# Kernel tuning notes

Hardware: AMD Instinct MI355X
Metric: run time of the kernel (lower is better)

## Reference

```python
import jax, jax.numpy as jnp
import numpy as np

B, S, M = 32, 512, 8
DF = 512          # per-feature dim (face/fc/img/label)
DIM1 = 4 * DF     # 2048
DIM2 = 512        # memory dim / hidden dim
EPS = 1e-05


def setup_inputs() -> dict:
    key = jax.random.key(0)
    ks = jax.random.split(key, 10)
    def g(k, shape, scale=1.0):
        return jax.random.normal(k, shape, dtype=jnp.float32) * scale
    fc_feat = g(ks[0], (B, S, DF))
    img_feat = g(ks[1], (B, S, DF))
    label_feat = g(ks[2], (B, DF))
    memory = g(ks[3], (B, M, DIM2))
    face = g(ks[4], (B, S, DF))
    face_mask = jax.random.randint(ks[5], (B, S), 0, 2).astype(jnp.float32)
    # params: linear1 (dim1+dim2 -> dim2) with bias, linear2 (dim2 -> 1) no bias
    xav1 = (2.0 / (DIM1 + DIM2 + DIM2)) ** 0.5
    xav2 = (2.0 / (DIM2 + 1)) ** 0.5
    W1 = g(ks[6], (DIM2, DIM1 + DIM2), xav1)
    b1 = jnp.zeros((DIM2,), dtype=jnp.float32)
    w2 = g(ks[7], (DIM2,), xav2)
    return {"fc_feat": fc_feat, "img_feat": img_feat, "label_feat": label_feat,
            "memory": memory, "face": face, "face_mask": face_mask,
            "W1": W1, "b1": b1, "w2": w2}


def reference(fc_feat, img_feat, label_feat, memory, face, face_mask, W1, b1, w2):
    b, s, _ = face.shape
    m = memory.shape[1]
    # concat along feature dim of (face, fc, img, label) -> [B,S,DIM1]
    base = jnp.concatenate(
        [face, fc_feat, img_feat,
         jnp.broadcast_to(label_feat[:, None, :], (b, s, label_feat.shape[-1]))],
        axis=-1)
    # linear1 split: W1 @ cat(base, mem) = W1a@base + W1b@mem  (avoids B*M*S*(dim1+dim2) concat)
    part_base = jnp.einsum('bsd,hd->bsh', base, W1[:, :DIM1])      # [B,S,H]
    part_mem = jnp.einsum('bmd,hd->bmh', memory, W1[:, DIM1:])     # [B,M,H]
    h = jnp.tanh(part_base[:, None, :, :] + part_mem[:, :, None, :] + b1)  # [B,M,S,H]
    e = jnp.einsum('bmsh,h->bms', h, w2).reshape(b, m * s)         # memory-major flatten
    alpha = jax.nn.softmax(e, axis=1)
    final_mask = jnp.tile(face_mask, (1, m))                       # face_mask.repeat(1, M)
    alpha = alpha * final_mask
    alpha = alpha / (alpha.sum(axis=1, keepdims=True) + EPS)
    # bmm(alpha, face.repeat(1,M,1)) == sum over m,s of alpha * face
    context = jnp.einsum('bms,bsd->bd', alpha.reshape(b, m, s), face)
    return alpha, context
```

## Files before the change

### kernel.cpp

```cpp
#include <hip/hip_runtime.h>
#include <hip/hip_bf16.h>
#include <math.h>

#define NB 32
#define NS 512
#define NM 8
#define NH 512
#define WSTRIDE 2560
#define FEPS 1e-5f

typedef __attribute__((ext_vector_type(4))) float f32x4;
typedef __attribute__((ext_vector_type(8))) short bf16x8;
typedef __attribute__((ext_vector_type(8))) unsigned short ushort8;

__device__ __forceinline__ unsigned short f2b(float f) {
  union { __hip_bfloat16 h; unsigned short u; } cv;
  cv.h = __float2bfloat16(f);
  return cv.u;
}

#define LDSK 40

template<int KSTEPS>
__global__ __launch_bounds__(256, 4)
void gemm_base_kernel(const float* __restrict__ face,
                      const float* __restrict__ fcf,
                      const float* __restrict__ imgf,
                      const float* __restrict__ labf,
                      const float* __restrict__ W1,
                      float* __restrict__ pb)
{
  __shared__ unsigned short As[2][128 * LDSK];
  __shared__ unsigned short Bs[2][128 * LDSK];

  const int tid  = threadIdx.x;
  const int lane = tid & 63;
  const int wid  = tid >> 6;
  const int wr   = wid >> 1;
  const int wc   = wid & 1;

  const int bid = blockIdx.x;
  const int cpx = gridDim.x >> 3;
  const int sid = (bid & 7) * cpx + (bid >> 3);
  const int kk   = sid >> 9;
  const int blkm = (sid >> 2) & 127;
  const int blkn = sid & 3;

  const int r  = tid >> 1;
  const int ch = (tid & 1) << 4;

  const int gr = blkm * 128 + r;
  const int bb = gr >> 9;
  const int gh = blkn * 128 + r;

  const int rl = lane & 15;
  const int kq = (lane >> 4) << 3;

  f32x4 acc[4][4];
  #pragma unroll
  for (int i = 0; i < 4; ++i)
    #pragma unroll
    for (int j = 0; j < 4; ++j)
      acc[i][j] = (f32x4){0.f, 0.f, 0.f, 0.f};

  float ra[16], rb[16];

#define LOAD_REGS(KTG) do {                                                 \
    const int kt_ = (KTG);                                                  \
    const int off_ = ((kt_ & 15) << 5) | ch;                                \
    const int reg_ = kt_ >> 4;                                              \
    const float* pa_;                                                       \
    if      (reg_ == 0) pa_ = face + (size_t)gr * 512 + off_;               \
    else if (reg_ == 1) pa_ = fcf  + (size_t)gr * 512 + off_;               \
    else if (reg_ == 2) pa_ = imgf + (size_t)gr * 512 + off_;               \
    else                pa_ = labf + (size_t)bb * 512 + off_;               \
    const float* pw_ = W1 + (size_t)gh * WSTRIDE + (kt_ << 5) + ch;         \
    _Pragma("unroll")                                                       \
    for (int i_ = 0; i_ < 4; ++i_) {                                        \
      f32x4 va_ = *(const f32x4*)(pa_ + 4 * i_);                            \
      f32x4 vb_ = *(const f32x4*)(pw_ + 4 * i_);                            \
      ra[4*i_+0] = va_[0]; ra[4*i_+1] = va_[1];                             \
      ra[4*i_+2] = va_[2]; ra[4*i_+3] = va_[3];                             \
      rb[4*i_+0] = vb_[0]; rb[4*i_+1] = vb_[1];                             \
      rb[4*i_+2] = vb_[2]; rb[4*i_+3] = vb_[3];                             \
    }                                                                       \
  } while (0)

#define WRITE_LDS(BUF) do {                                                 \
    ushort8 a0_, a1_, b0_, b1_;                                             \
    _Pragma("unroll")                                                       \
    for (int j_ = 0; j_ < 8; ++j_) {                                        \
      a0_[j_] = f2b(ra[j_]);   a1_[j_] = f2b(ra[8 + j_]);                   \
      b0_[j_] = f2b(rb[j_]);   b1_[j_] = f2b(rb[8 + j_]);                   \
    }                                                                       \
    *(ushort8*)&As[BUF][r * LDSK + ch]     = a0_;                           \
    *(ushort8*)&As[BUF][r * LDSK + ch + 8] = a1_;                           \
    *(ushort8*)&Bs[BUF][r * LDSK + ch]     = b0_;                           \
    *(ushort8*)&Bs[BUF][r * LDSK + ch + 8] = b1_;                           \
  } while (0)

#define COMPUTE(BUF) do {                                                   \
    bf16x8 af_[4], bf_[4];                                                  \
    _Pragma("unroll")                                                       \
    for (int m_ = 0; m_ < 4; ++m_)                                          \
      af_[m_] = *(const bf16x8*)&As[BUF][(wr*64 + m_*16 + rl) * LDSK + kq]; \
    _Pragma("unroll")                                                       \
    for (int n_ = 0; n_ < 4; ++n_)                                          \
      bf_[n_] = *(const bf16x8*)&Bs[BUF][(wc*64 + n_*16 + rl) * LDSK + kq]; \
    _Pragma("unroll")                                                       \
    for (int m_ = 0; m_ < 4; ++m_)                                          \
      _Pragma("unroll")                                                     \
      for (int n_ = 0; n_ < 4; ++n_)                                        \
        acc[m_][n_] = __builtin_amdgcn_mfma_f32_16x16x32_bf16(              \
            af_[m_], bf_[n_], acc[m_][n_], 0, 0, 0);                        \
  } while (0)

  const int kbase = kk * 32;
  LOAD_REGS(kbase);
  WRITE_LDS(0);
  __syncthreads();

  int buf = 0;
  #pragma unroll 1
  for (int kt = 0; kt < KSTEPS; ++kt) {
    if (kt < KSTEPS - 1) LOAD_REGS(kbase + kt + 1);
    COMPUTE(buf);
    if (kt < KSTEPS - 1) WRITE_LDS(buf ^ 1);
    __syncthreads();
    buf ^= 1;
  }

  float* pbo = pb + (size_t)kk * ((size_t)NB * NS * 512);
  const int crow = blkm * 128 + wr * 64;
  const int ccol = blkn * 128 + wc * 64 + rl;
  #pragma unroll
  for (int m = 0; m < 4; ++m)
    #pragma unroll
    for (int n = 0; n < 4; ++n)
      #pragma unroll
      for (int j = 0; j < 4; ++j) {
        const int row = crow + m * 16 + (lane >> 4) * 4 + j;
        pbo[(size_t)row * 512 + ccol + n * 16] = acc[m][n][j];
      }

#undef LOAD_REGS
#undef WRITE_LDS
#undef COMPUTE
}

__global__ __launch_bounds__(256)
void pm_kernel(const float* __restrict__ memory,
               const float* __restrict__ W1,
               const float* __restrict__ b1,
               float* __restrict__ pm)
{
  __shared__ float ms[NM * 512];
  const int b  = blockIdx.x;
  const int ht = blockIdx.y;
  const int t  = threadIdx.x;
  const int w  = t >> 6;
  const int l  = t & 63;

  const float* src = memory + (size_t)b * NM * 512;
  #pragma unroll
  for (int i = 0; i < 4; ++i)
    ((f32x4*)ms)[t + i * 256] = ((const f32x4*)src)[t + i * 256];
  __syncthreads();

  #pragma unroll 1
  for (int i = 0; i < 16; ++i) {
    const int h = ht * 64 + w * 16 + i;
    const float* wrow = W1 + (size_t)h * WSTRIDE + 2048;
    const f32x4 w0 = *(const f32x4*)(wrow + l * 4);
    const f32x4 w1 = *(const f32x4*)(wrow + 256 + l * 4);
    float part[NM];
    #pragma unroll
    for (int m = 0; m < NM; ++m) {
      const f32x4 m0 = *(const f32x4*)&ms[m * 512 + l * 4];
      const f32x4 m1 = *(const f32x4*)&ms[m * 512 + 256 + l * 4];
      part[m] = w0[0]*m0[0] + w0[1]*m0[1] + w0[2]*m0[2] + w0[3]*m0[3]
              + w1[0]*m1[0] + w1[1]*m1[1] + w1[2]*m1[2] + w1[3]*m1[3];
    }
    #pragma unroll
    for (int off = 32; off >= 1; off >>= 1)
      #pragma unroll
      for (int m = 0; m < NM; ++m)
        part[m] += __shfl_xor(part[m], off);
    if (l == 0) {
      const float bias = b1[h];
      #pragma unroll
      for (int m = 0; m < NM; ++m)
        pm[((size_t)b * NM + m) * 512 + h] = part[m] + bias;
    }
  }
}

template<int SPLIT>
__global__ __launch_bounds__(128)
void e_kernel(const float* __restrict__ pb0,
              const float* __restrict__ pb1,
              const float* __restrict__ pm,
              const float* __restrict__ w2,
              float* __restrict__ e)
{
  __shared__ float pbs[16 * 516];
  __shared__ float pms[NM * 516];
  __shared__ float w2s[512];

  const int b  = blockIdx.x;
  const int st = blockIdx.y;
  const int t  = threadIdx.x;

  const f32x4* s0 = (const f32x4*)(pb0 + ((size_t)b * NS + st * 16) * 512);
  const f32x4* s1 = (const f32x4*)(pb1 + ((size_t)b * NS + st * 16) * 512);
  #pragma unroll
  for (int i = 0; i < 16; ++i) {
    const int fi = t + i * 128;
    f32x4 v = s0[fi];
    if (SPLIT) {
      f32x4 v1 = s1[fi];
      v[0]+=v1[0]; v[1]+=v1[1]; v[2]+=v1[2]; v[3]+=v1[3];
    }
    const int f32i = fi * 4;
    *(f32x4*)&pbs[(f32i >> 9) * 516 + (f32i & 511)] = v;
  }
  const float* pmsrc = pm + (size_t)b * NM * 512;
  #pragma unroll
  for (int i = 0; i < 8; ++i) {
    const int fi = t + i * 128;
    f32x4 v = ((const f32x4*)pmsrc)[fi];
    const int f32i = fi * 4;
    *(f32x4*)&pms[(f32i >> 9) * 516 + (f32i & 511)] = v;
  }
  ((f32x4*)w2s)[t] = ((const f32x4*)w2)[t];
  __syncthreads();

  const int sl = t >> 3;
  const int m  = t & 7;
  const float* prow = &pbs[sl * 516];
  const float* mrow = &pms[m * 516];

  float acc = 0.f;
  for (int h = 0; h < 512; h += 4) {
    f32x4 pv = *(const f32x4*)&prow[h];
    f32x4 mv = *(const f32x4*)&mrow[h];
    f32x4 wv = *(const f32x4*)&w2s[h];
    #pragma unroll
    for (int j = 0; j < 4; ++j) {
      const float x  = pv[j] + mv[j];
      const float ex = __expf(x + x);
      const float th = 1.f - __fdividef(2.f, ex + 1.f);
      acc += wv[j] * th;
    }
  }
  e[(size_t)b * (NM * NS) + m * NS + st * 16 + sl] = acc;
}

__global__ __launch_bounds__(256)
void softmax_kernel(const float* __restrict__ e,
                    const float* __restrict__ face_mask,
                    float* __restrict__ out_alpha,
                    float* __restrict__ wsum)
{
  __shared__ float ev[NM * NS];
  __shared__ float msk[NS];
  __shared__ float redX[4], redA[4], redM[4];

  const int b = blockIdx.x;
  const int t = threadIdx.x;
  const int lane = t & 63;
  const int wv = t >> 6;

  const float* erow = e + (size_t)b * (NM * NS);
  #pragma unroll
  for (int i = 0; i < 4; ++i)
    ((f32x4*)ev)[t + i * 256] = ((const f32x4*)erow)[t + i * 256];
  if (t < 128)
    ((f32x4*)msk)[t] = ((const f32x4*)(face_mask + (size_t)b * NS))[t];
  __syncthreads();

  float mx = -3.402823466e38f;
  for (int i = t; i < NM * NS; i += 256) mx = fmaxf(mx, ev[i]);
  #pragma unroll
  for (int o = 32; o >= 1; o >>= 1) mx = fmaxf(mx, __shfl_xor(mx, o));
  if (lane == 0) redX[wv] = mx;
  __syncthreads();
  mx = fmaxf(fmaxf(redX[0], redX[1]), fmaxf(redX[2], redX[3]));

  float sA = 0.f, sM = 0.f;
  for (int i = t; i < NM * NS; i += 256) {
    const float p = __expf(ev[i] - mx);
    ev[i] = p;
    sA += p;
    sM += p * msk[i & 511];
  }
  #pragma unroll
  for (int o = 32; o >= 1; o >>= 1) {
    sA += __shfl_xor(sA, o);
    sM += __shfl_xor(sM, o);
  }
  if (lane == 0) { redA[wv] = sA; redM[wv] = sM; }
  __syncthreads();
  sA = redA[0] + redA[1] + redA[2] + redA[3];
  sM = redM[0] + redM[1] + redM[2] + redM[3];

  const float rr = sM / sA;
  const float scale = 1.f / (sA * (rr + FEPS));

  for (int i = t; i < NM * NS; i += 256) {
    const float a = ev[i] * msk[i & 511] * scale;
    ev[i] = a;
    out_alpha[(size_t)b * (NM * NS) + i] = a;
  }
  __syncthreads();

  for (int s = t; s < NS; s += 256) {
    float w = 0.f;
    #pragma unroll
    for (int m = 0; m < NM; ++m) w += ev[m * NS + s];
    wsum[(size_t)b * NS + s] = w;
  }
}

__global__ __launch_bounds__(128)
void ctx_kernel(const float* __restrict__ wsum,
                const float* __restrict__ face,
                float* __restrict__ out_ctx)
{
  const int b  = blockIdx.x;
  const int sq = blockIdx.y;
  const int t  = threadIdx.x;

  f32x4 acc = (f32x4){0.f, 0.f, 0.f, 0.f};
  const int s0 = sq * 64;
  #pragma unroll 4
  for (int si = 0; si < 64; ++si) {
    const int s = s0 + si;
    const float w = wsum[(size_t)b * NS + s];
    const f32x4 fv = ((const f32x4*)(face + ((size_t)b * NS + s) * 512))[t];
    acc[0] += w * fv[0]; acc[1] += w * fv[1];
    acc[2] += w * fv[2]; acc[3] += w * fv[3];
  }
  float* dst = out_ctx + (size_t)b * 512 + t * 4;
  atomicAdd(dst + 0, acc[0]);
  atomicAdd(dst + 1, acc[1]);
  atomicAdd(dst + 2, acc[2]);
  atomicAdd(dst + 3, acc[3]);
}

extern "C" void kernel_launch(void* const* d_in, const int* in_sizes, int n_in,
                              void* d_out, int out_size, void* d_ws, size_t ws_size,
                              hipStream_t stream)
{
  const float* fc_feat  = (const float*)d_in[0];
  const float* img_feat = (const float*)d_in[1];
  const float* label    = (const float*)d_in[2];
  const float* memory   = (const float*)d_in[3];
  const float* face     = (const float*)d_in[4];
  const float* fmask    = (const float*)d_in[5];
  const float* W1       = (const float*)d_in[6];
  const float* b1       = (const float*)d_in[7];
  const float* w2       = (const float*)d_in[8];

  float* out       = (float*)d_out;
  float* alpha_out = out;
  float* ctx_out   = out + (size_t)NB * NM * NS;

  const size_t szPB = (size_t)NB * NS * 512 * 4;
  const size_t szPM = (size_t)NB * NM * 512 * 4;
  const size_t szE  = (size_t)NB * NM * NS * 4;
  const size_t need_split = 2 * szPB + szPM + szE + (size_t)NB * NS * 4;
  const bool split = ws_size >= need_split;

  char* ws = (char*)d_ws;
  float* pb0 = (float*)ws;
  float* pb1 = split ? (float*)(ws + szPB) : pb0;
  char*  tail = ws + (split ? 2 * szPB : szPB);
  float* pm = (float*)tail;
  float* ee = (float*)(tail + szPM);
  float* wsum = (float*)(tail + szPM + szE);

  hipMemsetAsync(ctx_out, 0, (size_t)NB * 512 * 4, stream);

  if (split)
    gemm_base_kernel<32><<<1024, 256, 0, stream>>>(face, fc_feat, img_feat, label, W1, pb0);
  else
    gemm_base_kernel<64><<<512, 256, 0, stream>>>(face, fc_feat, img_feat, label, W1, pb0);

  pm_kernel<<<dim3(NB, 8), 256, 0, stream>>>(memory, W1, b1, pm);

  if (split)
    e_kernel<1><<<dim3(NB, NS / 16), 128, 0, stream>>>(pb0, pb1, pm, w2, ee);
  else
    e_kernel<0><<<dim3(NB, NS / 16), 128, 0, stream>>>(pb0, pb1, pm, w2, ee);

  softmax_kernel<<<NB, 256, 0, stream>>>(ee, fmask, alpha_out, wsum);
  ctx_kernel<<<dim3(NB, 8), 128, 0, stream>>>(wsum, face, ctx_out);
}
```

Before: 330.7 us.

## Replace split-K GEMM with 128x64 tiles and restructure e_kernel by H quarters

The base GEMM drops its split-K scheme, which wrote two partial output buffers that were summed later. It now uses 128x64 output tiles over the full K, so 1024 blocks are still launched with a single output buffer. The main loop holds two register sets for deeper prefetch. The e_kernel now splits the H dimension into four quarters per thread with padded LDS strides and combines them with shuffles, which raises thread parallelism and removes the pb1 read-and-add. The trade-off is that the A tile is reloaded twice as often per output column and each block runs a longer K loop, with launch bounds loosened to 3 blocks per CU.

```diff
diff --git a/kernel.cpp b/kernel.cpp
--- a/kernel.cpp
+++ b/kernel.cpp
@@ -21,8 +21,7 @@
 
 #define LDSK 40
 
-template<int KSTEPS>
-__global__ __launch_bounds__(256, 4)
+__global__ __launch_bounds__(256, 3)
 void gemm_base_kernel(const float* __restrict__ face,
                       const float* __restrict__ fcf,
                       const float* __restrict__ imgf,
@@ -31,7 +30,7 @@
                       float* __restrict__ pb)
 {
   __shared__ unsigned short As[2][128 * LDSK];
-  __shared__ unsigned short Bs[2][128 * LDSK];
+  __shared__ unsigned short Bs[2][64 * LDSK];
 
   const int tid  = threadIdx.x;
   const int lane = tid & 63;
@@ -42,109 +41,113 @@
   const int bid = blockIdx.x;
   const int cpx = gridDim.x >> 3;
   const int sid = (bid & 7) * cpx + (bid >> 3);
-  const int kk   = sid >> 9;
-  const int blkm = (sid >> 2) & 127;
-  const int blkn = sid & 3;
-
-  const int r  = tid >> 1;
-  const int ch = (tid & 1) << 4;
-
-  const int gr = blkm * 128 + r;
-  const int bb = gr >> 9;
-  const int gh = blkn * 128 + r;
+  const int blkm = sid >> 3;
+  const int blkn = sid & 7;
+
+  const int ar  = tid >> 1;
+  const int ach = (tid & 1) << 4;
+  const int br  = tid >> 2;
+  const int bch = (tid & 3) << 3;
+
+  const int gr = blkm * 128 + ar;
+  const int bb = blkm >> 2;
+  const int gh = blkn * 64 + br;
 
   const int rl = lane & 15;
   const int kq = (lane >> 4) << 3;
 
-  f32x4 acc[4][4];
+  f32x4 acc[4][2];
   #pragma unroll
   for (int i = 0; i < 4; ++i)
     #pragma unroll
-    for (int j = 0; j < 4; ++j)
+    for (int j = 0; j < 2; ++j)
       acc[i][j] = (f32x4){0.f, 0.f, 0.f, 0.f};
 
-  float ra[16], rb[16];
-
-#define LOAD_REGS(KTG) do {                                                 \
+  float raA[16], rbA[8], raB[16], rbB[8];
+
+#define LOADS(RA, RB, KTG) do {                                             \
     const int kt_ = (KTG);                                                  \
-    const int off_ = ((kt_ & 15) << 5) | ch;                                \
+    const int offA_ = ((kt_ & 15) << 5) | ach;                              \
     const int reg_ = kt_ >> 4;                                              \
     const float* pa_;                                                       \
-    if      (reg_ == 0) pa_ = face + (size_t)gr * 512 + off_;               \
-    else if (reg_ == 1) pa_ = fcf  + (size_t)gr * 512 + off_;               \
-    else if (reg_ == 2) pa_ = imgf + (size_t)gr * 512 + off_;               \
-    else                pa_ = labf + (size_t)bb * 512 + off_;               \
-    const float* pw_ = W1 + (size_t)gh * WSTRIDE + (kt_ << 5) + ch;         \
+    if      (reg_ == 0) pa_ = face + (size_t)gr * 512 + offA_;              \
+    else if (reg_ == 1) pa_ = fcf  + (size_t)gr * 512 + offA_;              \
+    else if (reg_ == 2) pa_ = imgf + (size_t)gr * 512 + offA_;              \
+    else                pa_ = labf + (size_t)bb * 512 + offA_;              \
     _Pragma("unroll")                                                       \
     for (int i_ = 0; i_ < 4; ++i_) {                                        \
       f32x4 va_ = *(const f32x4*)(pa_ + 4 * i_);                            \
+      RA[4*i_+0] = va_[0]; RA[4*i_+1] = va_[1];                             \
+      RA[4*i_+2] = va_[2]; RA[4*i_+3] = va_[3];                             \
+    }                                                                       \
+    const float* pw_ = W1 + (size_t)gh * WSTRIDE + (kt_ << 5) + bch;        \
+    _Pragma("unroll")                                                       \
+    for (int i_ = 0; i_ < 2; ++i_) {                                        \
       f32x4 vb_ = *(const f32x4*)(pw_ + 4 * i_);                            \
-      ra[4*i_+0] = va_[0]; ra[4*i_+1] = va_[1];                             \
-      ra[4*i_+2] = va_[2]; ra[4*i_+3] = va_[3];                             \
-      rb[4*i_+0] = vb_[0]; rb[4*i_+1] = vb_[1];                             \
-      rb[4*i_+2] = vb_[2]; rb[4*i_+3] = vb_[3];                             \
+      RB[4*i_+0] = vb_[0]; RB[4*i_+1] = vb_[1];                             \
+      RB[4*i_+2] = vb_[2]; RB[4*i_+3] = vb_[3];                             \
     }                                                                       \
   } while (0)
 
-#define WRITE_LDS(BUF) do {                                                 \
-    ushort8 a0_, a1_, b0_, b1_;                                             \
+#define WLDS(RA, RB, BUF) do {                                              \
+    ushort8 a0_, a1_, b0_;                                                  \
     _Pragma("unroll")                                                       \
     for (int j_ = 0; j_ < 8; ++j_) {                                        \
-      a0_[j_] = f2b(ra[j_]);   a1_[j_] = f2b(ra[8 + j_]);                   \
-      b0_[j_] = f2b(rb[j_]);   b1_[j_] = f2b(rb[8 + j_]);                   \
+      a0_[j_] = f2b(RA[j_]);   a1_[j_] = f2b(RA[8 + j_]);                   \
+      b0_[j_] = f2b(RB[j_]);                                                \
     }                                                                       \
-    *(ushort8*)&As[BUF][r * LDSK + ch]     = a0_;                           \
-    *(ushort8*)&As[BUF][r * LDSK + ch + 8] = a1_;                           \
-    *(ushort8*)&Bs[BUF][r * LDSK + ch]     = b0_;                           \
-    *(ushort8*)&Bs[BUF][r * LDSK + ch + 8] = b1_;                           \
+    *(ushort8*)&As[BUF][ar * LDSK + ach]     = a0_;                         \
+    *(ushort8*)&As[BUF][ar * LDSK + ach + 8] = a1_;                         \
+    *(ushort8*)&Bs[BUF][br * LDSK + bch]     = b0_;                         \
   } while (0)
 
 #define COMPUTE(BUF) do {                                                   \
-    bf16x8 af_[4], bf_[4];                                                  \
+    bf16x8 af_[4], bf_[2];                                                  \
     _Pragma("unroll")                                                       \
     for (int m_ = 0; m_ < 4; ++m_)                                          \
       af_[m_] = *(const bf16x8*)&As[BUF][(wr*64 + m_*16 + rl) * LDSK + kq]; \
     _Pragma("unroll")                                                       \
-    for (int n_ = 0; n_ < 4; ++n_)                                          \
-      bf_[n_] = *(const bf16x8*)&Bs[BUF][(wc*64 + n_*16 + rl) * LDSK + kq]; \
+    for (int n_ = 0; n_ < 2; ++n_)                                          \
+      bf_[n_] = *(const bf16x8*)&Bs[BUF][(wc*32 + n_*16 + rl) * LDSK + kq]; \
     _Pragma("unroll")                                                       \
     for (int m_ = 0; m_ < 4; ++m_)                                          \
       _Pragma("unroll")                                                     \
-      for (int n_ = 0; n_ < 4; ++n_)                                        \
+      for (int n_ = 0; n_ < 2; ++n_)                                        \
         acc[m_][n_] = __builtin_amdgcn_mfma_f32_16x16x32_bf16(              \
             af_[m_], bf_[n_], acc[m_][n_], 0, 0, 0);                        \
   } while (0)
 
-  const int kbase = kk * 32;
-  LOAD_REGS(kbase);
-  WRITE_LDS(0);
-  __syncthreads();
-
-  int buf = 0;
+  LOADS(raA, rbA, 0);
+  LOADS(raB, rbB, 1);
+  WLDS(raA, rbA, 0);
+  __syncthreads();
+
   #pragma unroll 1
-  for (int kt = 0; kt < KSTEPS; ++kt) {
-    if (kt < KSTEPS - 1) LOAD_REGS(kbase + kt + 1);
-    COMPUTE(buf);
-    if (kt < KSTEPS - 1) WRITE_LDS(buf ^ 1);
+  for (int kt = 0; kt < 64; kt += 2) {
+    if (kt + 2 < 64) LOADS(raA, rbA, kt + 2);
+    COMPUTE(0);
+    WLDS(raB, rbB, 1);
     __syncthreads();
-    buf ^= 1;
-  }
-
-  float* pbo = pb + (size_t)kk * ((size_t)NB * NS * 512);
+    if (kt + 3 < 64) LOADS(raB, rbB, kt + 3);
+    COMPUTE(1);
+    if (kt + 2 < 64) WLDS(raA, rbA, 0);
+    __syncthreads();
+  }
+
   const int crow = blkm * 128 + wr * 64;
-  const int ccol = blkn * 128 + wc * 64 + rl;
+  const int ccol = blkn * 64 + wc * 32 + rl;
   #pragma unroll
   for (int m = 0; m < 4; ++m)
     #pragma unroll
-    for (int n = 0; n < 4; ++n)
+    for (int n = 0; n < 2; ++n)
       #pragma unroll
       for (int j = 0; j < 4; ++j) {
         const int row = crow + m * 16 + (lane >> 4) * 4 + j;
-        pbo[(size_t)row * 512 + ccol + n * 16] = acc[m][n][j];
+        pb[(size_t)row * 512 + ccol + n * 16] = acc[m][n][j];
       }
 
-#undef LOAD_REGS
-#undef WRITE_LDS
+#undef LOADS
+#undef WLDS
 #undef COMPUTE
 }
 
@@ -195,65 +198,75 @@
   }
 }
 
-template<int SPLIT>
-__global__ __launch_bounds__(128)
-void e_kernel(const float* __restrict__ pb0,
-              const float* __restrict__ pb1,
+#define ERST 580
+#define EQST 144
+
+__global__ __launch_bounds__(256)
+void e_kernel(const float* __restrict__ pb,
               const float* __restrict__ pm,
               const float* __restrict__ w2,
               float* __restrict__ e)
 {
-  __shared__ float pbs[16 * 516];
-  __shared__ float pms[NM * 516];
-  __shared__ float w2s[512];
+  __shared__ float pbs[8 * ERST];
+  __shared__ float pms[8 * ERST];
+  __shared__ float w2s[4 * 136];
 
   const int b  = blockIdx.x;
   const int st = blockIdx.y;
   const int t  = threadIdx.x;
-
-  const f32x4* s0 = (const f32x4*)(pb0 + ((size_t)b * NS + st * 16) * 512);
-  const f32x4* s1 = (const f32x4*)(pb1 + ((size_t)b * NS + st * 16) * 512);
-  #pragma unroll
-  for (int i = 0; i < 16; ++i) {
-    const int fi = t + i * 128;
-    f32x4 v = s0[fi];
-    if (SPLIT) {
-      f32x4 v1 = s1[fi];
-      v[0]+=v1[0]; v[1]+=v1[1]; v[2]+=v1[2]; v[3]+=v1[3];
+  const int s0 = st * 8;
+
+  const f32x4* psrc = (const f32x4*)(pb + ((size_t)b * NS + s0) * 512);
+  #pragma unroll
+  for (int i = 0; i < 4; ++i) {
+    const int fi = t + i * 256;
+    const f32x4 v = psrc[fi];
+    const int f32i = fi * 4;
+    const int row = f32i >> 9, col = f32i & 511;
+    *(f32x4*)&pbs[row * ERST + (col >> 7) * EQST + (col & 127)] = v;
+  }
+  {
+    const f32x4* msrc = (const f32x4*)(pm + (size_t)b * NM * 512);
+    #pragma unroll
+    for (int i = 0; i < 4; ++i) {
+      const int fi = t + i * 256;
+      const f32x4 v = msrc[fi];
+      const int f32i = fi * 4;
+      const int row = f32i >> 9, col = f32i & 511;
+      *(f32x4*)&pms[row * ERST + (col >> 7) * EQST + (col & 127)] = v;
     }
-    const int f32i = fi * 4;
-    *(f32x4*)&pbs[(f32i >> 9) * 516 + (f32i & 511)] = v;
-  }
-  const float* pmsrc = pm + (size_t)b * NM * 512;
-  #pragma unroll
-  for (int i = 0; i < 8; ++i) {
-    const int fi = t + i * 128;
-    f32x4 v = ((const f32x4*)pmsrc)[fi];
-    const int f32i = fi * 4;
-    *(f32x4*)&pms[(f32i >> 9) * 516 + (f32i & 511)] = v;
-  }
-  ((f32x4*)w2s)[t] = ((const f32x4*)w2)[t];
-  __syncthreads();
-
-  const int sl = t >> 3;
-  const int m  = t & 7;
-  const float* prow = &pbs[sl * 516];
-  const float* mrow = &pms[m * 516];
+  }
+  if (t < 128) {
+    const f32x4 v = ((const f32x4*)w2)[t];
+    const int f32i = t * 4;
+    *(f32x4*)&w2s[(f32i >> 7) * 136 + (f32i & 127)] = v;
+  }
+  __syncthreads();
+
+  const int q  = t & 3;
+  const int m  = (t >> 2) & 7;
+  const int sl = t >> 5;
+  const float* prow = &pbs[sl * ERST + q * EQST];
+  const float* mrow = &pms[m * ERST + q * EQST];
+  const float* wq   = &w2s[q * 136];
 
   float acc = 0.f;
-  for (int h = 0; h < 512; h += 4) {
-    f32x4 pv = *(const f32x4*)&prow[h];
-    f32x4 mv = *(const f32x4*)&mrow[h];
-    f32x4 wv = *(const f32x4*)&w2s[h];
+  #pragma unroll 4
+  for (int hh = 0; hh < 128; hh += 4) {
+    const f32x4 pv = *(const f32x4*)&prow[hh];
+    const f32x4 mv = *(const f32x4*)&mrow[hh];
+    const f32x4 wv = *(const f32x4*)&wq[hh];
     #pragma unroll
     for (int j = 0; j < 4; ++j) {
       const float x  = pv[j] + mv[j];
       const float ex = __expf(x + x);
-      const float th = 1.f - __fdividef(2.f, ex + 1.f);
-      acc += wv[j] * th;
+      acc += wv[j] * (1.f - __fdividef(2.f, ex + 1.f));
     }
   }
-  e[(size_t)b * (NM * NS) + m * NS + st * 16 + sl] = acc;
+  acc += __shfl_xor(acc, 1);
+  acc += __shfl_xor(acc, 2);
+  if (q == 0)
+    e[(size_t)b * (NM * NS) + m * NS + s0 + sl] = acc;
 }
 
 __global__ __launch_bounds__(256)
@@ -369,31 +382,18 @@
   const size_t szPB = (size_t)NB * NS * 512 * 4;
   const size_t szPM = (size_t)NB * NM * 512 * 4;
   const size_t szE  = (size_t)NB * NM * NS * 4;
-  const size_t need_split = 2 * szPB + szPM + szE + (size_t)NB * NS * 4;
-  const bool split = ws_size >= need_split;
 
   char* ws = (char*)d_ws;
-  float* pb0 = (float*)ws;
-  float* pb1 = split ? (float*)(ws + szPB) : pb0;
-  char*  tail = ws + (split ? 2 * szPB : szPB);
-  float* pm = (float*)tail;
-  float* ee = (float*)(tail + szPM);
-  float* wsum = (float*)(tail + szPM + szE);
+  float* pb   = (float*)ws;
+  float* pm   = (float*)(ws + szPB);
+  float* ee   = (float*)(ws + szPB + szPM);
+  float* wsum = (float*)(ws + szPB + szPM + szE);
 
   hipMemsetAsync(ctx_out, 0, (size_t)NB * 512 * 4, stream);
 
-  if (split)
-    gemm_base_kernel<32><<<1024, 256, 0, stream>>>(face, fc_feat, img_feat, label, W1, pb0);
-  else
-    gemm_base_kernel<64><<<512, 256, 0, stream>>>(face, fc_feat, img_feat, label, W1, pb0);
-
+  gemm_base_kernel<<<1024, 256, 0, stream>>>(face, fc_feat, img_feat, label, W1, pb);
   pm_kernel<<<dim3(NB, 8), 256, 0, stream>>>(memory, W1, b1, pm);
-
-  if (split)
-    e_kernel<1><<<dim3(NB, NS / 16), 128, 0, stream>>>(pb0, pb1, pm, w2, ee);
-  else
-    e_kernel<0><<<dim3(NB, NS / 16), 128, 0, stream>>>(pb0, pb1, pm, w2, ee);
-
+  e_kernel<<<dim3(NB, NS / 8), 256, 0, stream>>>(pb, pm, w2, ee);
   softmax_kernel<<<NB, 256, 0, stream>>>(ee, fmask, alpha_out, wsum);
   ctx_kernel<<<dim3(NB, 8), 128, 0, stream>>>(wsum, face, ctx_out);
 }
```

Result: faster. 297.0 us (-10.2%).

## Stage GEMM tiles via direct global-to-LDS loads, drop split-K, streamline e_kernel

Applied to the files above, without the earlier changes.

The base GEMM now stages fp32 tiles straight into LDS with global_load_lds into an XOR-swizzled layout, and converts to bf16 when fragments are read, instead of loading into registers, converting and then writing LDS. The split-K variant and its second partial buffer are removed, so every launch uses 512 blocks over the full K and the e_kernel no longer sums two partials. The e_kernel reads pb rows directly from global memory rather than staging them in LDS, and uses 256 threads over 32 rows per block. The trade-off is double the LDS footprint for fp32 tiles, repeated bf16 conversion per fragment read, and fewer blocks in the GEMM.

```diff
diff --git a/kernel.cpp b/kernel.cpp
--- a/kernel.cpp
+++ b/kernel.cpp
@@ -11,7 +11,6 @@
 
 typedef __attribute__((ext_vector_type(4))) float f32x4;
 typedef __attribute__((ext_vector_type(8))) short bf16x8;
-typedef __attribute__((ext_vector_type(8))) unsigned short ushort8;
 
 __device__ __forceinline__ unsigned short f2b(float f) {
   union { __hip_bfloat16 h; unsigned short u; } cv;
@@ -19,10 +18,13 @@
   return cv.u;
 }
 
-#define LDSK 40
-
-template<int KSTEPS>
-__global__ __launch_bounds__(256, 4)
+__device__ __forceinline__ void gll16(const float* g, float* l) {
+  __builtin_amdgcn_global_load_lds(
+      (const __attribute__((address_space(1))) void*)g,
+      (__attribute__((address_space(3))) void*)l, 16, 0, 0);
+}
+
+__global__ __launch_bounds__(256)
 void gemm_base_kernel(const float* __restrict__ face,
                       const float* __restrict__ fcf,
                       const float* __restrict__ imgf,
@@ -30,8 +32,8 @@
                       const float* __restrict__ W1,
                       float* __restrict__ pb)
 {
-  __shared__ unsigned short As[2][128 * LDSK];
-  __shared__ unsigned short Bs[2][128 * LDSK];
+  __shared__ __align__(16) float Af[2][128 * 32];
+  __shared__ __align__(16) float Bf[2][128 * 32];
 
   const int tid  = threadIdx.x;
   const int lane = tid & 63;
@@ -42,19 +44,61 @@
   const int bid = blockIdx.x;
   const int cpx = gridDim.x >> 3;
   const int sid = (bid & 7) * cpx + (bid >> 3);
-  const int kk   = sid >> 9;
-  const int blkm = (sid >> 2) & 127;
+  const int blkm = sid >> 2;
   const int blkn = sid & 3;
-
-  const int r  = tid >> 1;
-  const int ch = (tid & 1) << 4;
-
-  const int gr = blkm * 128 + r;
-  const int bb = gr >> 9;
-  const int gh = blkn * 128 + r;
+  const int bb   = blkm >> 2;
 
   const int rl = lane & 15;
-  const int kq = (lane >> 4) << 3;
+  const int g2 = (lane >> 4) << 1;
+
+#define STAGE(BUF, KT) do {                                                  \
+    const int kt_ = (KT);                                                    \
+    const int seg_ = kt_ >> 4;                                               \
+    const int colf_ = (kt_ & 15) << 5;          \
+    _Pragma("unroll")                                                        \
+    for (int i_ = 0; i_ < 4; ++i_) {                                         \
+      const int c_   = tid + (i_ << 8);                                      \
+      const int row_ = c_ >> 3;                                              \
+      const int sw_  = ((c_ ^ row_) & 7) << 2;         \
+      const float* ga_;                                                      \
+      if (seg_ == 3)                                                         \
+        ga_ = labf + (size_t)bb * 512 + colf_ + sw_;                         \
+      else {                                                                 \
+        const float* ab_ = (seg_ == 0) ? face : (seg_ == 1) ? fcf : imgf;    \
+        ga_ = ab_ + (size_t)(blkm * 128 + row_) * 512 + colf_ + sw_;         \
+      }                                                                      \
+      const float* gb_ = W1 + (size_t)(blkn * 128 + row_) * WSTRIDE          \
+                            + (kt_ << 5) + sw_;                              \
+      const int cb_ = (c_ & ~63) << 2;          \
+      gll16(ga_, &Af[BUF][cb_]);                                             \
+      gll16(gb_, &Bf[BUF][cb_]);                                             \
+    }                                                                        \
+  } while (0)
+
+#define FRAG(DST, LP, ROW) do {                                              \
+    const int row_ = (ROW);                                                  \
+    const int ua_  = g2 ^ (row_ & 7);                                        \
+    const f32x4 h0_ = *(const f32x4*)&LP[row_ * 32 + ua_ * 4];               \
+    const f32x4 h1_ = *(const f32x4*)&LP[row_ * 32 + (ua_ ^ 1) * 4];         \
+    DST[0] = (short)f2b(h0_[0]); DST[1] = (short)f2b(h0_[1]);                \
+    DST[2] = (short)f2b(h0_[2]); DST[3] = (short)f2b(h0_[3]);                \
+    DST[4] = (short)f2b(h1_[0]); DST[5] = (short)f2b(h1_[1]);                \
+    DST[6] = (short)f2b(h1_[2]); DST[7] = (short)f2b(h1_[3]);                \
+  } while (0)
+
+#define COMPUTE(BUF) do {                                                    \
+    bf16x8 af_[4], bf_[4];                                                   \
+    _Pragma("unroll")                                                        \
+    for (int m_ = 0; m_ < 4; ++m_) FRAG(af_[m_], Af[BUF], wr*64 + m_*16 + rl);\
+    _Pragma("unroll")                                                        \
+    for (int n_ = 0; n_ < 4; ++n_) FRAG(bf_[n_], Bf[BUF], wc*64 + n_*16 + rl);\
+    _Pragma("unroll")                                                        \
+    for (int m_ = 0; m_ < 4; ++m_)                                           \
+      _Pragma("unroll")                                                      \
+      for (int n_ = 0; n_ < 4; ++n_)                                         \
+        acc[m_][n_] = __builtin_amdgcn_mfma_f32_16x16x32_bf16(               \
+            af_[m_], bf_[n_], acc[m_][n_], 0, 0, 0);                         \
+  } while (0)
 
   f32x4 acc[4][4];
   #pragma unroll
@@ -63,74 +107,18 @@
     for (int j = 0; j < 4; ++j)
       acc[i][j] = (f32x4){0.f, 0.f, 0.f, 0.f};
 
-  float ra[16], rb[16];
-
-#define LOAD_REGS(KTG) do {                                                 \
-    const int kt_ = (KTG);                                                  \
-    const int off_ = ((kt_ & 15) << 5) | ch;                                \
-    const int reg_ = kt_ >> 4;                                              \
-    const float* pa_;                                                       \
-    if      (reg_ == 0) pa_ = face + (size_t)gr * 512 + off_;               \
-    else if (reg_ == 1) pa_ = fcf  + (size_t)gr * 512 + off_;               \
-    else if (reg_ == 2) pa_ = imgf + (size_t)gr * 512 + off_;               \
-    else                pa_ = labf + (size_t)bb * 512 + off_;               \
-    const float* pw_ = W1 + (size_t)gh * WSTRIDE + (kt_ << 5) + ch;         \
-    _Pragma("unroll")                                                       \
-    for (int i_ = 0; i_ < 4; ++i_) {                                        \
-      f32x4 va_ = *(const f32x4*)(pa_ + 4 * i_);                            \
-      f32x4 vb_ = *(const f32x4*)(pw_ + 4 * i_);                            \
-      ra[4*i_+0] = va_[0]; ra[4*i_+1] = va_[1];                             \
-      ra[4*i_+2] = va_[2]; ra[4*i_+3] = va_[3];                             \
-      rb[4*i_+0] = vb_[0]; rb[4*i_+1] = vb_[1];                             \
-      rb[4*i_+2] = vb_[2]; rb[4*i_+3] = vb_[3];                             \
-    }                                                                       \
-  } while (0)
-
-#define WRITE_LDS(BUF) do {                                                 \
-    ushort8 a0_, a1_, b0_, b1_;                                             \
-    _Pragma("unroll")                                                       \
-    for (int j_ = 0; j_ < 8; ++j_) {                                        \
-      a0_[j_] = f2b(ra[j_]);   a1_[j_] = f2b(ra[8 + j_]);                   \
-      b0_[j_] = f2b(rb[j_]);   b1_[j_] = f2b(rb[8 + j_]);                   \
-    }                                                                       \
-    *(ushort8*)&As[BUF][r * LDSK + ch]     = a0_;                           \
-    *(ushort8*)&As[BUF][r * LDSK + ch + 8] = a1_;                           \
-    *(ushort8*)&Bs[BUF][r * LDSK + ch]     = b0_;                           \
-    *(ushort8*)&Bs[BUF][r * LDSK + ch + 8] = b1_;                           \
-  } while (0)
-
-#define COMPUTE(BUF) do {                                                   \
-    bf16x8 af_[4], bf_[4];                                                  \
-    _Pragma("unroll")                                                       \
-    for (int m_ = 0; m_ < 4; ++m_)                                          \
-      af_[m_] = *(const bf16x8*)&As[BUF][(wr*64 + m_*16 + rl) * LDSK + kq]; \
-    _Pragma("unroll")                                                       \
-    for (int n_ = 0; n_ < 4; ++n_)                                          \
-      bf_[n_] = *(const bf16x8*)&Bs[BUF][(wc*64 + n_*16 + rl) * LDSK + kq]; \
-    _Pragma("unroll")                                                       \
-    for (int m_ = 0; m_ < 4; ++m_)                                          \
-      _Pragma("unroll")                                                     \
-      for (int n_ = 0; n_ < 4; ++n_)                                        \
-        acc[m_][n_] = __builtin_amdgcn_mfma_f32_16x16x32_bf16(              \
-            af_[m_], bf_[n_], acc[m_][n_], 0, 0, 0);                        \
-  } while (0)
-
-  const int kbase = kk * 32;
-  LOAD_REGS(kbase);
-  WRITE_LDS(0);
+  STAGE(0, 0);
   __syncthreads();
 
   int buf = 0;
   #pragma unroll 1
-  for (int kt = 0; kt < KSTEPS; ++kt) {
-    if (kt < KSTEPS - 1) LOAD_REGS(kbase + kt + 1);
+  for (int kt = 0; kt < 64; ++kt) {
+    if (kt < 63) STAGE(buf ^ 1, kt + 1);
     COMPUTE(buf);
-    if (kt < KSTEPS - 1) WRITE_LDS(buf ^ 1);
     __syncthreads();
     buf ^= 1;
   }
 
-  float* pbo = pb + (size_t)kk * ((size_t)NB * NS * 512);
   const int crow = blkm * 128 + wr * 64;
   const int ccol = blkn * 128 + wc * 64 + rl;
   #pragma unroll
@@ -140,11 +128,11 @@
       #pragma unroll
       for (int j = 0; j < 4; ++j) {
         const int row = crow + m * 16 + (lane >> 4) * 4 + j;
-        pbo[(size_t)row * 512 + ccol + n * 16] = acc[m][n][j];
+        pb[(size_t)row * 512 + ccol + n * 16] = acc[m][n][j];
       }
 
-#undef LOAD_REGS
-#undef WRITE_LDS
+#undef STAGE
+#undef FRAG
 #undef COMPUTE
 }
 
@@ -195,65 +183,53 @@
   }
 }
 
-template<int SPLIT>
-__global__ __launch_bounds__(128)
-void e_kernel(const float* __restrict__ pb0,
-              const float* __restrict__ pb1,
+__global__ __launch_bounds__(256)
+void e_kernel(const float* __restrict__ pb,
               const float* __restrict__ pm,
               const float* __restrict__ w2,
               float* __restrict__ e)
 {
-  __shared__ float pbs[16 * 516];
-  __shared__ float pms[NM * 516];
+  __shared__ float pms[NM * 520];
   __shared__ float w2s[512];
 
   const int b  = blockIdx.x;
   const int st = blockIdx.y;
   const int t  = threadIdx.x;
 
-  const f32x4* s0 = (const f32x4*)(pb0 + ((size_t)b * NS + st * 16) * 512);
-  const f32x4* s1 = (const f32x4*)(pb1 + ((size_t)b * NS + st * 16) * 512);
-  #pragma unroll
-  for (int i = 0; i < 16; ++i) {
-    const int fi = t + i * 128;
-    f32x4 v = s0[fi];
-    if (SPLIT) {
-      f32x4 v1 = s1[fi];
-      v[0]+=v1[0]; v[1]+=v1[1]; v[2]+=v1[2]; v[3]+=v1[3];
+  {
+    const f32x4* msrc = (const f32x4*)(pm + (size_t)b * NM * 512);
+    #pragma unroll
+    for (int i = 0; i < 4; ++i) {
+      const int fi = t + i * 256;
+      const int row = fi >> 7, col = (fi & 127) << 2;
+      *(f32x4*)&pms[row * 520 + col] = msrc[fi];
     }
-    const int f32i = fi * 4;
-    *(f32x4*)&pbs[(f32i >> 9) * 516 + (f32i & 511)] = v;
-  }
-  const float* pmsrc = pm + (size_t)b * NM * 512;
-  #pragma unroll
-  for (int i = 0; i < 8; ++i) {
-    const int fi = t + i * 128;
-    f32x4 v = ((const f32x4*)pmsrc)[fi];
-    const int f32i = fi * 4;
-    *(f32x4*)&pms[(f32i >> 9) * 516 + (f32i & 511)] = v;
-  }
-  ((f32x4*)w2s)[t] = ((const f32x4*)w2)[t];
-  __syncthreads();
-
+  }
+  if (t < 128)
+    ((f32x4*)w2s)[t] = ((const f32x4*)w2)[t];
+  __syncthreads();
+
+  const int m  = t & 7;
   const int sl = t >> 3;
-  const int m  = t & 7;
-  const float* prow = &pbs[sl * 516];
-  const float* mrow = &pms[m * 516];
+  const int s  = st * 32 + sl;
+
+  const float* prow = pb + ((size_t)b * NS + s) * 512;
+  const float* mrow = &pms[m * 520];
 
   float acc = 0.f;
+  #pragma unroll 4
   for (int h = 0; h < 512; h += 4) {
-    f32x4 pv = *(const f32x4*)&prow[h];
-    f32x4 mv = *(const f32x4*)&mrow[h];
-    f32x4 wv = *(const f32x4*)&w2s[h];
+    const f32x4 pv = *(const f32x4*)&prow[h];
+    const f32x4 mv = *(const f32x4*)&mrow[h];
+    const f32x4 wv = *(const f32x4*)&w2s[h];
     #pragma unroll
     for (int j = 0; j < 4; ++j) {
       const float x  = pv[j] + mv[j];
       const float ex = __expf(x + x);
-      const float th = 1.f - __fdividef(2.f, ex + 1.f);
-      acc += wv[j] * th;
+      acc += wv[j] * (1.f - __fdividef(2.f, ex + 1.f));
     }
   }
-  e[(size_t)b * (NM * NS) + m * NS + st * 16 + sl] = acc;
+  e[(size_t)b * (NM * NS) + m * NS + s] = acc;
 }
 
 __global__ __launch_bounds__(256)
@@ -369,31 +345,18 @@
   const size_t szPB = (size_t)NB * NS * 512 * 4;
   const size_t szPM = (size_t)NB * NM * 512 * 4;
   const size_t szE  = (size_t)NB * NM * NS * 4;
-  const size_t need_split = 2 * szPB + szPM + szE + (size_t)NB * NS * 4;
-  const bool split = ws_size >= need_split;
 
   char* ws = (char*)d_ws;
-  float* pb0 = (float*)ws;
-  float* pb1 = split ? (float*)(ws + szPB) : pb0;
-  char*  tail = ws + (split ? 2 * szPB : szPB);
-  float* pm = (float*)tail;
-  float* ee = (float*)(tail + szPM);
-  float* wsum = (float*)(tail + szPM + szE);
+  float* pb   = (float*)ws;
+  float* pm   = (float*)(ws + szPB);
+  float* ee   = (float*)(ws + szPB + szPM);
+  float* wsum = (float*)(ws + szPB + szPM + szE);
 
   hipMemsetAsync(ctx_out, 0, (size_t)NB * 512 * 4, stream);
 
-  if (split)
-    gemm_base_kernel<32><<<1024, 256, 0, stream>>>(face, fc_feat, img_feat, label, W1, pb0);
-  else
-    gemm_base_kernel<64><<<512, 256, 0, stream>>>(face, fc_feat, img_feat, label, W1, pb0);
-
+  gemm_base_kernel<<<512, 256, 0, stream>>>(face, fc_feat, img_feat, label, W1, pb);
   pm_kernel<<<dim3(NB, 8), 256, 0, stream>>>(memory, W1, b1, pm);
-
-  if (split)
-    e_kernel<1><<<dim3(NB, NS / 16), 128, 0, stream>>>(pb0, pb1, pm, w2, ee);
-  else
-    e_kernel<0><<<dim3(NB, NS / 16), 128, 0, stream>>>(pb0, pb1, pm, w2, ee);
-
+  e_kernel<<<dim3(NB, 16), 256, 0, stream>>>(pb, pm, w2, ee);
   softmax_kernel<<<NB, 256, 0, stream>>>(ee, fmask, alpha_out, wsum);
   ctx_kernel<<<dim3(NB, 8), 128, 0, stream>>>(wsum, face, ctx_out);
 }
```

Result: faster. 287.0 us (-13.2%).
